# Optimization experiments

Hardware: AMD Instinct MI355X
Metric: run time of the kernel (lower is better)

The kernel has to match this reference:

```python
import jax, jax.numpy as jnp
import numpy as np

N = 100000  # nodes (== in_feats, one-hot id features)
E = 3200000  # edges
D = 64       # out_feats == review_feat dim


def setup_inputs() -> dict:
    key = jax.random.key(0)
    k = jax.random.split(key, 7)
    weight = jax.random.normal(k[0], (N, D), dtype=jnp.float32) * 0.05
    ps_w = jax.random.normal(k[1], (1, D), dtype=jnp.float32) * 0.1
    review_feat = jax.random.normal(k[2], (E, D), dtype=jnp.float32)
    cj = jax.random.uniform(k[3], (N, 1), dtype=jnp.float32)
    ci = jax.random.uniform(k[4], (N, 1), dtype=jnp.float32)
    src = jax.random.randint(k[5], (E,), 0, N, dtype=jnp.int32)
    dst = jax.random.randint(k[6], (E,), 0, N, dtype=jnp.int32)
    return {"weight": weight, "ps_w": ps_w, "review_feat": review_feat,
            "cj": cj, "ci": ci, "src": src, "dst": dst}


def reference(weight, ps_w, review_feat, cj, ci, src, dst):
    # feat = dot_or_identity(None, weight) = weight; dropout_rate=0 -> identity
    feat = weight * cj  # [N, D], degree-normalized src features
    # edge gate: sigmoid(Linear(review_feat)) -> [E, 1]
    pa = jax.nn.sigmoid(review_feat @ ps_w.T)  # [E, 1]
    # message = pa * src_h, then segment-sum to dst (fn.sum)
    msg = pa * feat[src]  # [E, D]
    h = jax.ops.segment_sum(msg, dst, num_segments=weight.shape[0])  # [N, D]
    return h * ci
```

## Files before the change

### kernel.cpp

```cpp
#include <hip/hip_runtime.h>
#include <hip/hip_fp16.h>


#define HIST_BLOCKS  256
#define WCJ_BLOCKS   512
#define GATE_BLOCKS  2048
#define MAXDEG       256

__global__ __launch_bounds__(256) void kZ_zero(unsigned* __restrict__ deg, int n)
{
    const int i = blockIdx.x * 256 + threadIdx.x;
    if (i < n) deg[i] = 0u;
}

__global__ __launch_bounds__(256) void kM_all(
    const float* __restrict__ review_feat,
    const float* __restrict__ ps_w,
    const float* __restrict__ weight,
    const float* __restrict__ cj,
    const int*   __restrict__ src,
    const int*   __restrict__ dst,
    float*       __restrict__ scale,
    unsigned*    __restrict__ deg,
    int2*        __restrict__ pairs2,
    __half*      __restrict__ wcj,
    int E, int N)
{
    if (blockIdx.x < HIST_BLOCKS) {
        const long long gsz = (long long)HIST_BLOCKS * 256;
        const long long t0  = (long long)blockIdx.x * 256 + threadIdx.x;
        for (long long b = t0; b < E; b += gsz * 4) {
            long long e[4];
            int d[4], s[4];
            #pragma unroll
            for (int u = 0; u < 4; ++u) {
                e[u] = b + u * gsz;
                const bool ok = e[u] < E;
                d[u] = ok ? dst[e[u]] : 0;
                s[u] = ok ? src[e[u]] : 0;
            }
            unsigned r[4];
            #pragma unroll
            for (int u = 0; u < 4; ++u)
                if (e[u] < E) r[u] = atomicAdd(&deg[d[u]], 1u);
            #pragma unroll
            for (int u = 0; u < 4; ++u)
                if (e[u] < E && r[u] < MAXDEG)
                    pairs2[(long long)d[u] * MAXDEG + r[u]] = make_int2(s[u], (int)e[u]);
        }
        return;
    }

    if (blockIdx.x < HIST_BLOCKS + WCJ_BLOCKS) {
        const long long tid = (long long)(blockIdx.x - HIST_BLOCKS) * 256 + threadIdx.x;
        const long long nthreads = (long long)WCJ_BLOCKS * 256;
        const long long nq = (long long)N * 8;
        for (long long i = tid; i < nq; i += nthreads) {
            const int n = (int)(i >> 3);
            const float4 w0 = reinterpret_cast<const float4*>(weight)[i * 2];
            const float4 w1 = reinterpret_cast<const float4*>(weight)[i * 2 + 1];
            const float c = cj[n];
            const unsigned r0 = (unsigned)__half_as_ushort(__float2half(w0.x * c))
                              | ((unsigned)__half_as_ushort(__float2half(w0.y * c)) << 16);
            const unsigned r1 = (unsigned)__half_as_ushort(__float2half(w0.z * c))
                              | ((unsigned)__half_as_ushort(__float2half(w0.w * c)) << 16);
            const unsigned r2 = (unsigned)__half_as_ushort(__float2half(w1.x * c))
                              | ((unsigned)__half_as_ushort(__float2half(w1.y * c)) << 16);
            const unsigned r3 = (unsigned)__half_as_ushort(__float2half(w1.z * c))
                              | ((unsigned)__half_as_ushort(__float2half(w1.w * c)) << 16);
            reinterpret_cast<uint4*>(wcj)[i] = make_uint4(r0, r1, r2, r3);
        }
        return;
    }

    const int bid   = blockIdx.x - (HIST_BLOCKS + WCJ_BLOCKS);
    const int lane  = threadIdx.x & 63;
    const int wib   = threadIdx.x >> 6;
    const int group = lane >> 4;
    const int sub   = lane & 15;
    const float4 pw = *reinterpret_cast<const float4*>(ps_w + sub * 4);

    const long long nwaves = (long long)GATE_BLOCKS * 4;
    for (long long w = (long long)bid * 4 + wib; w * 32 < E; w += nwaves) {
        const long long ebase = w * 32;
        float4 rv[8];
        #pragma unroll
        for (int u = 0; u < 8; ++u) {
            const long long e = ebase + u * 4 + group;
            rv[u] = (e < E) ? *reinterpret_cast<const float4*>(review_feat + e * 64 + sub * 4)
                            : make_float4(0.f, 0.f, 0.f, 0.f);
        }
        float x[8];
        #pragma unroll
        for (int u = 0; u < 8; ++u) {
            float t = rv[u].x * pw.x + rv[u].y * pw.y + rv[u].z * pw.z + rv[u].w * pw.w;
            t += __shfl_xor(t, 1);
            t += __shfl_xor(t, 2);
            t += __shfl_xor(t, 4);
            t += __shfl_xor(t, 8);
            x[u] = t;
        }
        if (sub == 0) {
            #pragma unroll
            for (int u = 0; u < 8; ++u) {
                const long long e = ebase + u * 4 + group;
                if (e < E) scale[e] = 1.f / (1.f + __expf(-x[u]));
            }
        }
    }
}

__global__ __launch_bounds__(256, 4) void k5_gather(
    const __half*   __restrict__ wcj,
    const float*    __restrict__ ci,
    const float*    __restrict__ scale,
    const unsigned* __restrict__ deg,
    const int2*     __restrict__ pairs2,
    float*          __restrict__ out,
    int N)
{
    const int lane  = threadIdx.x & 63;
    const int wib   = threadIdx.x >> 6;
    const int group = lane >> 4;
    const int sub   = lane & 15;

    const long long n = ((long long)blockIdx.x * 4 + wib) * 4 + group;
    const bool valid = (n < N);

    unsigned cnt = 0;
    if (valid) {
        cnt = deg[n];
        if (cnt > MAXDEG) cnt = MAXDEG;
    }
    const long long base = n * (long long)MAXDEG;

    int2  p  = make_int2(0, 0);
    float sc16 = 0.f;
    if (sub < cnt) {
        p = pairs2[base + sub];
        sc16 = scale[p.y];
    }

    float4 acc = make_float4(0.f, 0.f, 0.f, 0.f);
    for (unsigned k0 = 0; __any((int)(k0 < cnt)); k0 += 16) {
        int2  pn  = make_int2(0, 0);
        float scn = 0.f;
        const unsigned nk = k0 + 16;
        if (nk + sub < cnt) {
            pn = pairs2[base + nk + sub];
            scn = scale[pn.y];
        }

        int m = (int)cnt - (int)k0;
        if (m > 16) m = 16;
        #pragma unroll 8
        for (int j = 0; j < m; ++j) {
            const int   s = __shfl(p.x, (group << 4) + j);
            const float g = __shfl(sc16, (group << 4) + j);
            const uint2 raw = *reinterpret_cast<const uint2*>(
                wcj + (long long)s * 64 + sub * 4);
            acc.x += g * __half2float(__ushort_as_half((unsigned short)(raw.x & 0xffffu)));
            acc.y += g * __half2float(__ushort_as_half((unsigned short)(raw.x >> 16)));
            acc.z += g * __half2float(__ushort_as_half((unsigned short)(raw.y & 0xffffu)));
            acc.w += g * __half2float(__ushort_as_half((unsigned short)(raw.y >> 16)));
        }
        p = pn;
        sc16 = scn;
    }
    if (valid) {
        const float c = ci[n];
        *reinterpret_cast<float4*>(out + n * 64 + sub * 4) =
            make_float4(acc.x * c, acc.y * c, acc.z * c, acc.w * c);
    }
}

extern "C" void kernel_launch(void* const* d_in, const int* in_sizes, int n_in,
                              void* d_out, int out_size, void* d_ws, size_t ws_size,
                              hipStream_t stream) {
    const float* weight      = (const float*)d_in[0];
    const float* ps_w        = (const float*)d_in[1];
    const float* review_feat = (const float*)d_in[2];
    const float* cj          = (const float*)d_in[3];
    const float* ci          = (const float*)d_in[4];
    const int*   src         = (const int*)d_in[5];
    const int*   dst         = (const int*)d_in[6];
    float*       out         = (float*)d_out;

    const int N = in_sizes[3];
    const int E = in_sizes[5];

    size_t off = 0;
    auto take = [&](size_t bytes) { size_t o = off; off = (off + bytes + 255) & ~(size_t)255; return o; };
    const size_t pairs2_o = take((size_t)N * MAXDEG * 8);
    const size_t scale_o  = take((size_t)E * 4);
    const size_t wcj_o    = take((size_t)N * 64 * 2);
    const size_t deg_o    = take((size_t)N * 4);

    char* base = (char*)d_ws;
    int2*     pairs2 = (int2*)    (base + pairs2_o);
    float*    scale  = (float*)   (base + scale_o);
    __half*   wcj    = (__half*)  (base + wcj_o);
    unsigned* deg    = (unsigned*)(base + deg_o);

    kZ_zero<<<(N + 255) / 256, 256, 0, stream>>>(deg, N);
    kM_all<<<HIST_BLOCKS + WCJ_BLOCKS + GATE_BLOCKS, 256, 0, stream>>>(
        review_feat, ps_w, weight, cj, src, dst, scale, deg, pairs2, wcj, E, N);
    const int blocksD = (N + 15) / 16;
    k5_gather<<<blocksD, 256, 0, stream>>>(wcj, ci, scale, deg, pairs2, out, N);
}
```

Measured before the change: 381.3 us.

## Pack source id and quantized gate into one word before gather

Splits the fused pass so the histogram records per-edge ranks while gate values are computed. A new scatter kernel then writes a single 32-bit word per edge that packs the source id (17 bits) with a 15-bit quantized sigmoid gate. This removes the random scale[e] load from the gather loop and halves the size of the pairs array. The cost is an extra kernel launch, extra rank read/write traffic and a re-read of src/dst, plus reduced gate precision from the 15-bit quantization. The packing also only works while N fits in 17 bits.

```diff
diff --git a/kernel.cpp b/kernel.cpp
--- a/kernel.cpp
+++ b/kernel.cpp
@@ -3,9 +3,10 @@
 
 
 #define HIST_BLOCKS  256
+#define GATE_BLOCKS  2048
 #define WCJ_BLOCKS   512
-#define GATE_BLOCKS  2048
 #define MAXDEG       256
+#define GATE_Q       32767.0f
 
 __global__ __launch_bounds__(256) void kZ_zero(unsigned* __restrict__ deg, int n)
 {
@@ -13,31 +14,25 @@
     if (i < n) deg[i] = 0u;
 }
 
-__global__ __launch_bounds__(256) void kM_all(
+__global__ __launch_bounds__(256) void kM_hist_gate(
     const float* __restrict__ review_feat,
     const float* __restrict__ ps_w,
-    const float* __restrict__ weight,
-    const float* __restrict__ cj,
-    const int*   __restrict__ src,
     const int*   __restrict__ dst,
     float*       __restrict__ scale,
+    unsigned*    __restrict__ rank,
     unsigned*    __restrict__ deg,
-    int2*        __restrict__ pairs2,
-    __half*      __restrict__ wcj,
-    int E, int N)
+    int E)
 {
     if (blockIdx.x < HIST_BLOCKS) {
         const long long gsz = (long long)HIST_BLOCKS * 256;
         const long long t0  = (long long)blockIdx.x * 256 + threadIdx.x;
         for (long long b = t0; b < E; b += gsz * 4) {
             long long e[4];
-            int d[4], s[4];
+            int d[4];
             #pragma unroll
             for (int u = 0; u < 4; ++u) {
                 e[u] = b + u * gsz;
-                const bool ok = e[u] < E;
-                d[u] = ok ? dst[e[u]] : 0;
-                s[u] = ok ? src[e[u]] : 0;
+                d[u] = (e[u] < E) ? dst[e[u]] : 0;
             }
             unsigned r[4];
             #pragma unroll
@@ -45,14 +40,61 @@
                 if (e[u] < E) r[u] = atomicAdd(&deg[d[u]], 1u);
             #pragma unroll
             for (int u = 0; u < 4; ++u)
-                if (e[u] < E && r[u] < MAXDEG)
-                    pairs2[(long long)d[u] * MAXDEG + r[u]] = make_int2(s[u], (int)e[u]);
+                if (e[u] < E) rank[e[u]] = r[u];
         }
         return;
     }
 
-    if (blockIdx.x < HIST_BLOCKS + WCJ_BLOCKS) {
-        const long long tid = (long long)(blockIdx.x - HIST_BLOCKS) * 256 + threadIdx.x;
+    const int bid   = blockIdx.x - HIST_BLOCKS;
+    const int lane  = threadIdx.x & 63;
+    const int wib   = threadIdx.x >> 6;
+    const int group = lane >> 4;
+    const int sub   = lane & 15;
+    const float4 pw = *reinterpret_cast<const float4*>(ps_w + sub * 4);
+
+    const long long nwaves = (long long)GATE_BLOCKS * 4;
+    for (long long w = (long long)bid * 4 + wib; w * 32 < E; w += nwaves) {
+        const long long ebase = w * 32;
+        float4 rv[8];
+        #pragma unroll
+        for (int u = 0; u < 8; ++u) {
+            const long long e = ebase + u * 4 + group;
+            rv[u] = (e < E) ? *reinterpret_cast<const float4*>(review_feat + e * 64 + sub * 4)
+                            : make_float4(0.f, 0.f, 0.f, 0.f);
+        }
+        float x[8];
+        #pragma unroll
+        for (int u = 0; u < 8; ++u) {
+            float t = rv[u].x * pw.x + rv[u].y * pw.y + rv[u].z * pw.z + rv[u].w * pw.w;
+            t += __shfl_xor(t, 1);
+            t += __shfl_xor(t, 2);
+            t += __shfl_xor(t, 4);
+            t += __shfl_xor(t, 8);
+            x[u] = t;
+        }
+        if (sub == 0) {
+            #pragma unroll
+            for (int u = 0; u < 8; ++u) {
+                const long long e = ebase + u * 4 + group;
+                if (e < E) scale[e] = 1.f / (1.f + __expf(-x[u]));
+            }
+        }
+    }
+}
+
+__global__ __launch_bounds__(256) void k4_scatter_wcj(
+    const int*      __restrict__ src,
+    const int*      __restrict__ dst,
+    const float*    __restrict__ scale,
+    const unsigned* __restrict__ rank,
+    unsigned*       __restrict__ pairs,
+    const float*    __restrict__ weight,
+    const float*    __restrict__ cj,
+    __half*         __restrict__ wcj,
+    int E, int N)
+{
+    if (blockIdx.x < WCJ_BLOCKS) {
+        const long long tid = (long long)blockIdx.x * 256 + threadIdx.x;
         const long long nthreads = (long long)WCJ_BLOCKS * 256;
         const long long nq = (long long)N * 8;
         for (long long i = tid; i < nq; i += nthreads) {
@@ -73,56 +115,43 @@
         return;
     }
 
-    const int bid   = blockIdx.x - (HIST_BLOCKS + WCJ_BLOCKS);
+    const long long gsz = (long long)(gridDim.x - WCJ_BLOCKS) * 256;
+    const long long t0  = (long long)(blockIdx.x - WCJ_BLOCKS) * 256 + threadIdx.x;
+
+    long long e[8];
+    int s[8], d[8];
+    float sc[8];
+    unsigned r[8];
+    #pragma unroll
+    for (int u = 0; u < 8; ++u) {
+        e[u] = t0 + u * gsz;
+        const bool ok = e[u] < E;
+        s[u]  = ok ? src[e[u]]   : 0;
+        d[u]  = ok ? dst[e[u]]   : 0;
+        sc[u] = ok ? scale[e[u]] : 0.f;
+        r[u]  = ok ? rank[e[u]]  : 0u;
+    }
+    #pragma unroll
+    for (int u = 0; u < 8; ++u) {
+        if (e[u] < E && r[u] < MAXDEG) {
+            const unsigned q = (unsigned)(sc[u] * GATE_Q + 0.5f);
+            pairs[(long long)d[u] * MAXDEG + r[u]] = ((unsigned)s[u] << 15) | q;
+        }
+    }
+}
+
+__global__ __launch_bounds__(256, 4) void k5_gather(
+    const __half*   __restrict__ wcj,
+    const float*    __restrict__ ci,
+    const unsigned* __restrict__ deg,
+    const unsigned* __restrict__ pairs,
+    float*          __restrict__ out,
+    int N)
+{
     const int lane  = threadIdx.x & 63;
     const int wib   = threadIdx.x >> 6;
     const int group = lane >> 4;
     const int sub   = lane & 15;
-    const float4 pw = *reinterpret_cast<const float4*>(ps_w + sub * 4);
-
-    const long long nwaves = (long long)GATE_BLOCKS * 4;
-    for (long long w = (long long)bid * 4 + wib; w * 32 < E; w += nwaves) {
-        const long long ebase = w * 32;
-        float4 rv[8];
-        #pragma unroll
-        for (int u = 0; u < 8; ++u) {
-            const long long e = ebase + u * 4 + group;
-            rv[u] = (e < E) ? *reinterpret_cast<const float4*>(review_feat + e * 64 + sub * 4)
-                            : make_float4(0.f, 0.f, 0.f, 0.f);
-        }
-        float x[8];
-        #pragma unroll
-        for (int u = 0; u < 8; ++u) {
-            float t = rv[u].x * pw.x + rv[u].y * pw.y + rv[u].z * pw.z + rv[u].w * pw.w;
-            t += __shfl_xor(t, 1);
-            t += __shfl_xor(t, 2);
-            t += __shfl_xor(t, 4);
-            t += __shfl_xor(t, 8);
-            x[u] = t;
-        }
-        if (sub == 0) {
-            #pragma unroll
-            for (int u = 0; u < 8; ++u) {
-                const long long e = ebase + u * 4 + group;
-                if (e < E) scale[e] = 1.f / (1.f + __expf(-x[u]));
-            }
-        }
-    }
-}
-
-__global__ __launch_bounds__(256, 4) void k5_gather(
-    const __half*   __restrict__ wcj,
-    const float*    __restrict__ ci,
-    const float*    __restrict__ scale,
-    const unsigned* __restrict__ deg,
-    const int2*     __restrict__ pairs2,
-    float*          __restrict__ out,
-    int N)
-{
-    const int lane  = threadIdx.x & 63;
-    const int wib   = threadIdx.x >> 6;
-    const int group = lane >> 4;
-    const int sub   = lane & 15;
 
     const long long n = ((long long)blockIdx.x * 4 + wib) * 4 + group;
     const bool valid = (n < N);
@@ -134,38 +163,30 @@
     }
     const long long base = n * (long long)MAXDEG;
 
-    int2  p  = make_int2(0, 0);
-    float sc16 = 0.f;
-    if (sub < cnt) {
-        p = pairs2[base + sub];
-        sc16 = scale[p.y];
-    }
+    unsigned p = 0;
+    if (sub < cnt) p = pairs[base + sub];
 
     float4 acc = make_float4(0.f, 0.f, 0.f, 0.f);
     for (unsigned k0 = 0; __any((int)(k0 < cnt)); k0 += 16) {
-        int2  pn  = make_int2(0, 0);
-        float scn = 0.f;
+        unsigned pn = 0;
         const unsigned nk = k0 + 16;
-        if (nk + sub < cnt) {
-            pn = pairs2[base + nk + sub];
-            scn = scale[pn.y];
-        }
+        if (nk + sub < cnt) pn = pairs[base + nk + sub];
 
         int m = (int)cnt - (int)k0;
         if (m > 16) m = 16;
         #pragma unroll 8
         for (int j = 0; j < m; ++j) {
-            const int   s = __shfl(p.x, (group << 4) + j);
-            const float g = __shfl(sc16, (group << 4) + j);
+            const unsigned pj = __shfl(p, (group << 4) + j);
+            const int   s  = (int)(pj >> 15);
+            const float sc = (float)(pj & 0x7fffu) * (1.0f / GATE_Q);
             const uint2 raw = *reinterpret_cast<const uint2*>(
                 wcj + (long long)s * 64 + sub * 4);
-            acc.x += g * __half2float(__ushort_as_half((unsigned short)(raw.x & 0xffffu)));
-            acc.y += g * __half2float(__ushort_as_half((unsigned short)(raw.x >> 16)));
-            acc.z += g * __half2float(__ushort_as_half((unsigned short)(raw.y & 0xffffu)));
-            acc.w += g * __half2float(__ushort_as_half((unsigned short)(raw.y >> 16)));
+            acc.x += sc * __half2float(__ushort_as_half((unsigned short)(raw.x & 0xffffu)));
+            acc.y += sc * __half2float(__ushort_as_half((unsigned short)(raw.x >> 16)));
+            acc.z += sc * __half2float(__ushort_as_half((unsigned short)(raw.y & 0xffffu)));
+            acc.w += sc * __half2float(__ushort_as_half((unsigned short)(raw.y >> 16)));
         }
         p = pn;
-        sc16 = scn;
     }
     if (valid) {
         const float c = ci[n];
@@ -191,20 +212,25 @@
 
     size_t off = 0;
     auto take = [&](size_t bytes) { size_t o = off; off = (off + bytes + 255) & ~(size_t)255; return o; };
-    const size_t pairs2_o = take((size_t)N * MAXDEG * 8);
-    const size_t scale_o  = take((size_t)E * 4);
-    const size_t wcj_o    = take((size_t)N * 64 * 2);
-    const size_t deg_o    = take((size_t)N * 4);
+    const size_t pairs_o = take((size_t)N * MAXDEG * 4);
+    const size_t scale_o = take((size_t)E * 4);
+    const size_t rank_o  = take((size_t)E * 4);
+    const size_t wcj_o   = take((size_t)N * 64 * 2);
+    const size_t deg_o   = take((size_t)N * 4);
 
     char* base = (char*)d_ws;
-    int2*     pairs2 = (int2*)    (base + pairs2_o);
-    float*    scale  = (float*)   (base + scale_o);
-    __half*   wcj    = (__half*)  (base + wcj_o);
-    unsigned* deg    = (unsigned*)(base + deg_o);
+    unsigned* pairs = (unsigned*)(base + pairs_o);
+    float*    scale = (float*)   (base + scale_o);
+    unsigned* rank  = (unsigned*)(base + rank_o);
+    __half*   wcj   = (__half*)  (base + wcj_o);
+    unsigned* deg   = (unsigned*)(base + deg_o);
 
     kZ_zero<<<(N + 255) / 256, 256, 0, stream>>>(deg, N);
-    kM_all<<<HIST_BLOCKS + WCJ_BLOCKS + GATE_BLOCKS, 256, 0, stream>>>(
-        review_feat, ps_w, weight, cj, src, dst, scale, deg, pairs2, wcj, E, N);
+    kM_hist_gate<<<HIST_BLOCKS + GATE_BLOCKS, 256, 0, stream>>>(
+        review_feat, ps_w, dst, scale, rank, deg, E);
+    const int scatterBlocks = (int)(((long long)E + 8LL * 256 - 1) / (8LL * 256));
+    k4_scatter_wcj<<<WCJ_BLOCKS + scatterBlocks, 256, 0, stream>>>(
+        src, dst, scale, rank, pairs, weight, cj, wcj, E, N);
     const int blocksD = (N + 15) / 16;
-    k5_gather<<<blocksD, 256, 0, stream>>>(wcj, ci, scale, deg, pairs2, out, N);
-}
+    k5_gather<<<blocksD, 256, 0, stream>>>(wcj, ci, deg, pairs, out, N);
+}
```

After: 349.0 us. 1.09x faster.
